# Performance work log

Hardware: AMD Instinct MI355X
Metric: run time of the kernel (lower is better)

## Reference

```python
import jax, jax.numpy as jnp
import numpy as np

T = 1024       # context time steps
F = 2048       # number of features (independent chains)
LATENT = 128   # latent_dim
ODE_H = 256    # ode_hidden_dim


def setup_inputs() -> dict:
    key = jax.random.key(0)
    ks = jax.random.split(key, 12)
    # strictly increasing observation times in [0, 100]
    context_times = jnp.sort(jax.random.uniform(ks[0], (T,), jnp.float32)) * 100.0
    context_values = jax.random.normal(ks[1], (T, F), jnp.float32)
    context_mask = (jax.random.uniform(ks[2], (T, F), jnp.float32) < 0.7).astype(jnp.float32)
    s = 0.05
    # EncoderODEFunc: Linear(LATENT->ODE_H), Tanh, Linear(ODE_H->LATENT)
    W1 = jax.random.normal(ks[3], (ODE_H, LATENT), jnp.float32) * s
    b1 = jax.random.normal(ks[4], (ODE_H,), jnp.float32) * s
    W2 = jax.random.normal(ks[5], (LATENT, ODE_H), jnp.float32) * s
    b2 = jax.random.normal(ks[6], (LATENT,), jnp.float32) * s
    # GRUCell(input_size=1, hidden_size=LATENT); torch gate order: r, z, n
    W_ih = jax.random.normal(ks[7], (3 * LATENT, 1), jnp.float32) * s
    b_ih = jax.random.normal(ks[8], (3 * LATENT,), jnp.float32) * s
    W_hh = jax.random.normal(ks[9], (3 * LATENT, LATENT), jnp.float32) * s
    b_hh = jax.random.normal(ks[10], (3 * LATENT,), jnp.float32) * s
    return {"context_times": context_times, "context_values": context_values,
            "context_mask": context_mask, "W1": W1, "b1": b1, "W2": W2, "b2": b2,
            "W_ih": W_ih, "b_ih": b_ih, "W_hh": W_hh, "b_hh": b_hh}


def reference(context_times, context_values, context_mask,
              W1, b1, W2, b2, W_ih, b_ih, W_hh, b_hh):
    latent = W_hh.shape[1]
    rev_t = context_times[::-1]
    rev_v = context_values[::-1]        # [T, F]
    rev_m = context_mask[::-1]          # [T, F]
    # dt for step k (k>=1) = rev_t[k-1] - rev_t[k]; step 0 has no ODE solve
    dts = jnp.concatenate([jnp.zeros((1,), rev_t.dtype), rev_t[:-1] - rev_t[1:]])

    def ode_f(h):  # [F, latent] -> [F, latent]
        return jnp.tanh(h @ W1.T + b1) @ W2.T + b2

    def gru_cell(x, h):  # x: [F, 1], h: [F, latent]
        gi = x @ W_ih.T + b_ih          # [F, 3*latent]
        gh = h @ W_hh.T + b_hh
        ir, iz, inn = jnp.split(gi, 3, axis=-1)
        hr, hz, hn = jnp.split(gh, 3, axis=-1)
        r = jax.nn.sigmoid(ir + hr)
        z = jax.nn.sigmoid(iz + hz)
        n = jnp.tanh(inn + r * hn)
        return (1.0 - z) * n + z * h

    def step(h, inp):
        dt, obs, m = inp
        # single fixed Euler step over [0, dt] (torchdiffeq odeint, method='euler')
        h_ode = h + dt * ode_f(h)
        h = jnp.where(dt > 0.0, h_ode, h)
        h_cand = gru_cell(obs[:, None], h)
        m = m[:, None]
        return m * h_cand + (1.0 - m) * h, None

    h0 = jnp.zeros((context_values.shape[-1], latent), context_values.dtype)
    h, _ = jax.lax.scan(step, h0, (dts, rev_v, rev_m))
    return h  # [F, latent] == z0
```

## Files before the change

kernel.cpp:

```cpp
#include <hip/hip_runtime.h>

#define T_STEPS 1024
#define FDIM    2048
#define LAT     128
#define HID     256
#define MB      8
#define NTHR    512
#define NBLK    (FDIM / MB)

typedef __attribute__((ext_vector_type(8))) short bf16x8;
typedef __attribute__((ext_vector_type(4))) float f32x4;

#define L2E  1.4426950408889634f
#define C2E  2.8853900817779268f

__device__ __forceinline__ float exp2_(float x) {
#if __has_builtin(__builtin_amdgcn_exp2f)
    return __builtin_amdgcn_exp2f(x);
#else
    return __expf(0.6931471805599453f * x);
#endif
}
__device__ __forceinline__ float rcp_(float x) { return __builtin_amdgcn_rcpf(x); }

__device__ __forceinline__ unsigned short f2bu(float x) {
    unsigned u = __float_as_uint(x);
    u += 0x7fffu + ((u >> 16) & 1u);
    return (unsigned short)(u >> 16);
}
__device__ __forceinline__ short f2b(float x) { return (short)f2bu(x); }
__device__ __forceinline__ unsigned pk2(float a, float b) {
    return (unsigned)f2bu(a) | ((unsigned)f2bu(b) << 16);
}
__device__ __forceinline__ float2 pick2(f32x4 v, int hf) {
    float a = hf ? v[2] : v[0];
    float b = hf ? v[3] : v[1];
    return make_float2(a, b);
}


__global__ __launch_bounds__(NTHR, 2)
void odernn_kernel(const float* __restrict__ times,
                   const float* __restrict__ vals,
                   const float* __restrict__ mask,
                   const float* __restrict__ W1,  const float* __restrict__ b1,
                   const float* __restrict__ W2,  const float* __restrict__ b2,
                   const float* __restrict__ W_ih, const float* __restrict__ b_ih,
                   const float* __restrict__ Whh, const float* __restrict__ b_hh,
                   float* __restrict__ out)
{
    __shared__ float dts_s[T_STEPS];
    __shared__ short hTpre[16 * 64];
    __shared__ short hTpost[16 * 64];
    __shared__ short uT[32 * 64];

    const int tid = threadIdx.x;
    const int w   = tid >> 6;
    const int ln  = tid & 63;
    const int col = ln & 15;
    const int qd  = ln >> 4;
    const int m8  = ln & 7;
    const int hf  = (ln >> 3) & 1;
    const int fbase = blockIdx.x * MB;
    const int rbase = qd * 64 + m8 * 8;

    for (int e = tid; e < T_STEPS; e += NTHR)
        dts_s[e] = (e == 0) ? 0.0f : (times[T_STEPS - e] - times[T_STEPS - 1 - e]);
    for (int e = tid; e < 16 * 64; e += NTHR) { hTpre[e] = 0; hTpost[e] = 0; }

    auto loadW = [&](const float* __restrict__ W, int K, int tb, int kb) -> bf16x8 {
        const float* p = W + (size_t)(tb + col) * K + kb * 32 + qd * 8;
        const float4 a = *(const float4*)p;
        const float4 b = *(const float4*)(p + 4);
        bf16x8 r;
        r[0] = f2b(a.x); r[1] = f2b(a.y); r[2] = f2b(a.z); r[3] = f2b(a.w);
        r[4] = f2b(b.x); r[5] = f2b(b.y); r[6] = f2b(b.z); r[7] = f2b(b.w);
        return r;
    };

    bf16x8 w1a[2][4];
    #pragma unroll
    for (int i = 0; i < 2; ++i)
        #pragma unroll
        for (int kb = 0; kb < 4; ++kb) w1a[i][kb] = loadW(W1, LAT, (2 * w + i) * 16, kb);
    bf16x8 w2a[8];
    #pragma unroll
    for (int kb = 0; kb < 8; ++kb) w2a[kb] = loadW(W2, HID, w * 16, kb);
    bf16x8 wha[3][4];
    #pragma unroll
    for (int g = 0; g < 3; ++g)
        #pragma unroll
        for (int kb = 0; kb < 4; ++kb)
            wha[g][kb] = loadW(Whh, LAT, g * 128 + w * 16, kb);

    float cb1L[2][2], b2L[2];
    float wrS[2], brS[2], wzS[2], bzS[2], wnC[2], bnC[2], bhnC[2];
    #pragma unroll
    for (int i = 0; i < 2; ++i)
        #pragma unroll
        for (int j = 0; j < 2; ++j)
            cb1L[i][j] = C2E * b1[(2 * w + i) * 16 + qd * 4 + hf * 2 + j];
    #pragma unroll
    for (int j = 0; j < 2; ++j) {
        const int c = w * 16 + qd * 4 + hf * 2 + j;
        b2L[j]  = b2[c];
        wrS[j]  = -L2E * W_ih[c];
        brS[j]  = -L2E * (b_ih[c] + b_hh[c]);
        wzS[j]  = -L2E * W_ih[128 + c];
        bzS[j]  = -L2E * (b_ih[128 + c] + b_hh[128 + c]);
        wnC[j]  =  C2E * W_ih[256 + c];
        bnC[j]  =  C2E * b_ih[256 + c];
        bhnC[j] =  C2E * b_hh[256 + c];
    }
    float hreg[2] = {0.f, 0.f};
    const int myAddr = (w * 2 + (qd >> 1)) * 64 + m8 * 8 + (qd & 1) * 4 + hf * 2;

    const float* vp = vals + (size_t)(T_STEPS - 1) * FDIM + fbase + m8;
    const float* mp = mask + (size_t)(T_STEPS - 1) * FDIM + fbase + m8;

    __syncthreads();

    for (int t = 0; t < T_STEPS; ++t) {
        const float dt = dts_s[t];
        const float x  = *vp;  vp -= FDIM;
        const float mk = *mp;  mp -= FDIM;

        f32x4 a1[2] = {{0,0,0,0},{0,0,0,0}};
        #pragma unroll
        for (int kb = 0; kb < 4; ++kb) {
            const bf16x8 bf = *(const bf16x8*)(hTpre + kb * 256 + rbase);
            #pragma unroll
            for (int i = 0; i < 2; ++i)
                a1[i] = __builtin_amdgcn_mfma_f32_16x16x32_bf16(w1a[i][kb], bf, a1[i], 0, 0, 0);
        }
        #pragma unroll
        for (int i = 0; i < 2; ++i) {
            const float2 p = pick2(a1[i], hf);
            const float v0 = fmaf(-2.f, rcp_(1.f + exp2_(fmaf(p.x, C2E, cb1L[i][0]))), 1.f);
            const float v1 = fmaf(-2.f, rcp_(1.f + exp2_(fmaf(p.y, C2E, cb1L[i][1]))), 1.f);
            const int addr = ((2 * w + i) * 2 + (qd >> 1)) * 64 + m8 * 8 + (qd & 1) * 4 + hf * 2;
            *(unsigned*)(uT + addr) = pk2(v0, v1);
        }
        __syncthreads();

        f32x4 a2a = {0,0,0,0}, a2b = {0,0,0,0};
        #pragma unroll
        for (int kb = 0; kb < 4; ++kb) {
            const bf16x8 bfa = *(const bf16x8*)(uT + kb * 256 + rbase);
            const bf16x8 bfb = *(const bf16x8*)(uT + (kb + 4) * 256 + rbase);
            a2a = __builtin_amdgcn_mfma_f32_16x16x32_bf16(w2a[kb],     bfa, a2a, 0, 0, 0);
            a2b = __builtin_amdgcn_mfma_f32_16x16x32_bf16(w2a[kb + 4], bfb, a2b, 0, 0, 0);
        }
        {
            const f32x4 a2 = a2a + a2b;
            const float2 p = pick2(a2, hf);
            hreg[0] = fmaf(dt, p.x + b2L[0], hreg[0]);
            hreg[1] = fmaf(dt, p.y + b2L[1], hreg[1]);
            *(unsigned*)(hTpost + myAddr) = pk2(hreg[0], hreg[1]);
        }
        __syncthreads();

        f32x4 a3[3] = {{0,0,0,0},{0,0,0,0},{0,0,0,0}};
        #pragma unroll
        for (int kb = 0; kb < 4; ++kb) {
            const bf16x8 bf = *(const bf16x8*)(hTpost + kb * 256 + rbase);
            #pragma unroll
            for (int g = 0; g < 3; ++g)
                a3[g] = __builtin_amdgcn_mfma_f32_16x16x32_bf16(wha[g][kb], bf, a3[g], 0, 0, 0);
        }
        {
            const float2 gR = pick2(a3[0], hf);
            const float2 gZ = pick2(a3[1], hf);
            const float2 gN = pick2(a3[2], hf);
            const float gRv[2] = {gR.x, gR.y}, gZv[2] = {gZ.x, gZ.y}, gNv[2] = {gN.x, gN.y};
            #pragma unroll
            for (int j = 0; j < 2; ++j) {
                const float sr = rcp_(1.f + exp2_(fmaf(gRv[j], -L2E, fmaf(x, wrS[j], brS[j]))));
                const float sz = rcp_(1.f + exp2_(fmaf(gZv[j], -L2E, fmaf(x, wzS[j], bzS[j]))));
                const float yn = fmaf(sr, fmaf(gNv[j], C2E, bhnC[j]), fmaf(x, wnC[j], bnC[j]));
                const float nn = fmaf(-2.f, rcp_(1.f + exp2_(yn)), 1.f);
                const float hv = hreg[j];
                const float hc = fmaf(sz, hv - nn, nn);
                hreg[j] = fmaf(mk, hc - hv, hv);
            }
            *(unsigned*)(hTpre + myAddr) = pk2(hreg[0], hreg[1]);
        }
        __syncthreads();
    }

    {
        float2 o = make_float2(hreg[0], hreg[1]);
        *(float2*)(out + (size_t)(fbase + m8) * LAT + w * 16 + qd * 4 + hf * 2) = o;
    }
}

extern "C" void kernel_launch(void* const* d_in, const int* in_sizes, int n_in,
                              void* d_out, int out_size, void* d_ws, size_t ws_size,
                              hipStream_t stream) {
    const float* times = (const float*)d_in[0];
    const float* vals  = (const float*)d_in[1];
    const float* mask  = (const float*)d_in[2];
    const float* W1    = (const float*)d_in[3];
    const float* b1    = (const float*)d_in[4];
    const float* W2    = (const float*)d_in[5];
    const float* b2    = (const float*)d_in[6];
    const float* W_ih  = (const float*)d_in[7];
    const float* b_ih  = (const float*)d_in[8];
    const float* Whh   = (const float*)d_in[9];
    const float* b_hh  = (const float*)d_in[10];
    float* out = (float*)d_out;

    odernn_kernel<<<NBLK, NTHR, 0, stream>>>(times, vals, mask,
                                             W1, b1, W2, b2,
                                             W_ih, b_ih, Whh, b_hh, out);
}
```

Measured before the change: 1.124 ms.

## Halve waves per block and give each wave two output tiles

Cuts the block from 8 waves to 4 and has each wave compute twice as many 16-row tiles in every GEMM stage (W1, W2, W_hh). Weight fragments and per-column constants move into registers at twice the previous size. Launch bounds change to one block per SM. The aim is to cut barrier cost and wave count per serial time step and to give each wave more independent MFMAs to interleave. The cost is higher register pressure and fewer resident waves to hide latency.

```diff
diff --git a/kernel.cpp b/kernel.cpp
--- a/kernel.cpp
+++ b/kernel.cpp
@@ -5,7 +5,7 @@
 #define LAT     128
 #define HID     256
 #define MB      8
-#define NTHR    512
+#define NTHR    256
 #define NBLK    (FDIM / MB)
 
 typedef __attribute__((ext_vector_type(8))) short bf16x8;
@@ -39,7 +39,7 @@
 }
 
 
-__global__ __launch_bounds__(NTHR, 2)
+__global__ __launch_bounds__(NTHR, 1)
 void odernn_kernel(const float* __restrict__ times,
                    const float* __restrict__ vals,
                    const float* __restrict__ mask,
@@ -78,42 +78,51 @@
         return r;
     };
 
-    bf16x8 w1a[2][4];
+    bf16x8 w1a[4][4];
+    #pragma unroll
+    for (int i = 0; i < 4; ++i)
+        #pragma unroll
+        for (int kb = 0; kb < 4; ++kb) w1a[i][kb] = loadW(W1, LAT, (4 * w + i) * 16, kb);
+    bf16x8 w2a[2][8];
     #pragma unroll
     for (int i = 0; i < 2; ++i)
         #pragma unroll
-        for (int kb = 0; kb < 4; ++kb) w1a[i][kb] = loadW(W1, LAT, (2 * w + i) * 16, kb);
-    bf16x8 w2a[8];
-    #pragma unroll
-    for (int kb = 0; kb < 8; ++kb) w2a[kb] = loadW(W2, HID, w * 16, kb);
-    bf16x8 wha[3][4];
+        for (int kb = 0; kb < 8; ++kb) w2a[i][kb] = loadW(W2, HID, (2 * w + i) * 16, kb);
+    bf16x8 wha[3][2][4];
     #pragma unroll
     for (int g = 0; g < 3; ++g)
         #pragma unroll
-        for (int kb = 0; kb < 4; ++kb)
-            wha[g][kb] = loadW(Whh, LAT, g * 128 + w * 16, kb);
-
-    float cb1L[2][2], b2L[2];
-    float wrS[2], brS[2], wzS[2], bzS[2], wnC[2], bnC[2], bhnC[2];
+        for (int i = 0; i < 2; ++i)
+            #pragma unroll
+            for (int kb = 0; kb < 4; ++kb)
+                wha[g][i][kb] = loadW(Whh, LAT, g * 128 + (2 * w + i) * 16, kb);
+
+    float cb1L[4][2], b2L[2][2];
+    float wrS[2][2], brS[2][2], wzS[2][2], bzS[2][2], wnC[2][2], bnC[2][2], bhnC[2][2];
+    #pragma unroll
+    for (int i = 0; i < 4; ++i)
+        #pragma unroll
+        for (int j = 0; j < 2; ++j)
+            cb1L[i][j] = C2E * b1[(4 * w + i) * 16 + qd * 4 + hf * 2 + j];
     #pragma unroll
     for (int i = 0; i < 2; ++i)
         #pragma unroll
-        for (int j = 0; j < 2; ++j)
-            cb1L[i][j] = C2E * b1[(2 * w + i) * 16 + qd * 4 + hf * 2 + j];
-    #pragma unroll
-    for (int j = 0; j < 2; ++j) {
-        const int c = w * 16 + qd * 4 + hf * 2 + j;
-        b2L[j]  = b2[c];
-        wrS[j]  = -L2E * W_ih[c];
-        brS[j]  = -L2E * (b_ih[c] + b_hh[c]);
-        wzS[j]  = -L2E * W_ih[128 + c];
-        bzS[j]  = -L2E * (b_ih[128 + c] + b_hh[128 + c]);
-        wnC[j]  =  C2E * W_ih[256 + c];
-        bnC[j]  =  C2E * b_ih[256 + c];
-        bhnC[j] =  C2E * b_hh[256 + c];
-    }
-    float hreg[2] = {0.f, 0.f};
-    const int myAddr = (w * 2 + (qd >> 1)) * 64 + m8 * 8 + (qd & 1) * 4 + hf * 2;
+        for (int j = 0; j < 2; ++j) {
+            const int c = (2 * w + i) * 16 + qd * 4 + hf * 2 + j;
+            b2L[i][j]  = b2[c];
+            wrS[i][j]  = -L2E * W_ih[c];
+            brS[i][j]  = -L2E * (b_ih[c] + b_hh[c]);
+            wzS[i][j]  = -L2E * W_ih[128 + c];
+            bzS[i][j]  = -L2E * (b_ih[128 + c] + b_hh[128 + c]);
+            wnC[i][j]  =  C2E * W_ih[256 + c];
+            bnC[i][j]  =  C2E * b_ih[256 + c];
+            bhnC[i][j] =  C2E * b_hh[256 + c];
+        }
+    float hreg[2][2] = {{0.f, 0.f}, {0.f, 0.f}};
+    int myAddr[2];
+    #pragma unroll
+    for (int i = 0; i < 2; ++i)
+        myAddr[i] = ((2 * w + i) * 2 + (qd >> 1)) * 64 + m8 * 8 + (qd & 1) * 4 + hf * 2;
 
     const float* vp = vals + (size_t)(T_STEPS - 1) * FDIM + fbase + m8;
     const float* mp = mask + (size_t)(T_STEPS - 1) * FDIM + fbase + m8;
@@ -125,72 +134,80 @@
         const float x  = *vp;  vp -= FDIM;
         const float mk = *mp;  mp -= FDIM;
 
-        f32x4 a1[2] = {{0,0,0,0},{0,0,0,0}};
+        f32x4 a1[4] = {{0,0,0,0},{0,0,0,0},{0,0,0,0},{0,0,0,0}};
         #pragma unroll
         for (int kb = 0; kb < 4; ++kb) {
             const bf16x8 bf = *(const bf16x8*)(hTpre + kb * 256 + rbase);
             #pragma unroll
-            for (int i = 0; i < 2; ++i)
+            for (int i = 0; i < 4; ++i)
                 a1[i] = __builtin_amdgcn_mfma_f32_16x16x32_bf16(w1a[i][kb], bf, a1[i], 0, 0, 0);
         }
         #pragma unroll
-        for (int i = 0; i < 2; ++i) {
+        for (int i = 0; i < 4; ++i) {
             const float2 p = pick2(a1[i], hf);
             const float v0 = fmaf(-2.f, rcp_(1.f + exp2_(fmaf(p.x, C2E, cb1L[i][0]))), 1.f);
             const float v1 = fmaf(-2.f, rcp_(1.f + exp2_(fmaf(p.y, C2E, cb1L[i][1]))), 1.f);
-            const int addr = ((2 * w + i) * 2 + (qd >> 1)) * 64 + m8 * 8 + (qd & 1) * 4 + hf * 2;
+            const int addr = ((4 * w + i) * 2 + (qd >> 1)) * 64 + m8 * 8 + (qd & 1) * 4 + hf * 2;
             *(unsigned*)(uT + addr) = pk2(v0, v1);
         }
         __syncthreads();
 
-        f32x4 a2a = {0,0,0,0}, a2b = {0,0,0,0};
+        f32x4 a2a[2] = {{0,0,0,0},{0,0,0,0}}, a2b[2] = {{0,0,0,0},{0,0,0,0}};
         #pragma unroll
         for (int kb = 0; kb < 4; ++kb) {
             const bf16x8 bfa = *(const bf16x8*)(uT + kb * 256 + rbase);
             const bf16x8 bfb = *(const bf16x8*)(uT + (kb + 4) * 256 + rbase);
-            a2a = __builtin_amdgcn_mfma_f32_16x16x32_bf16(w2a[kb],     bfa, a2a, 0, 0, 0);
-            a2b = __builtin_amdgcn_mfma_f32_16x16x32_bf16(w2a[kb + 4], bfb, a2b, 0, 0, 0);
-        }
-        {
-            const f32x4 a2 = a2a + a2b;
+            #pragma unroll
+            for (int i = 0; i < 2; ++i) {
+                a2a[i] = __builtin_amdgcn_mfma_f32_16x16x32_bf16(w2a[i][kb],     bfa, a2a[i], 0, 0, 0);
+                a2b[i] = __builtin_amdgcn_mfma_f32_16x16x32_bf16(w2a[i][kb + 4], bfb, a2b[i], 0, 0, 0);
+            }
+        }
+        #pragma unroll
+        for (int i = 0; i < 2; ++i) {
+            const f32x4 a2 = a2a[i] + a2b[i];
             const float2 p = pick2(a2, hf);
-            hreg[0] = fmaf(dt, p.x + b2L[0], hreg[0]);
-            hreg[1] = fmaf(dt, p.y + b2L[1], hreg[1]);
-            *(unsigned*)(hTpost + myAddr) = pk2(hreg[0], hreg[1]);
+            hreg[i][0] = fmaf(dt, p.x + b2L[i][0], hreg[i][0]);
+            hreg[i][1] = fmaf(dt, p.y + b2L[i][1], hreg[i][1]);
+            *(unsigned*)(hTpost + myAddr[i]) = pk2(hreg[i][0], hreg[i][1]);
         }
         __syncthreads();
 
-        f32x4 a3[3] = {{0,0,0,0},{0,0,0,0},{0,0,0,0}};
+        f32x4 a3[3][2] = {{{0,0,0,0},{0,0,0,0}},{{0,0,0,0},{0,0,0,0}},{{0,0,0,0},{0,0,0,0}}};
         #pragma unroll
         for (int kb = 0; kb < 4; ++kb) {
             const bf16x8 bf = *(const bf16x8*)(hTpost + kb * 256 + rbase);
             #pragma unroll
             for (int g = 0; g < 3; ++g)
-                a3[g] = __builtin_amdgcn_mfma_f32_16x16x32_bf16(wha[g][kb], bf, a3[g], 0, 0, 0);
-        }
-        {
-            const float2 gR = pick2(a3[0], hf);
-            const float2 gZ = pick2(a3[1], hf);
-            const float2 gN = pick2(a3[2], hf);
+                #pragma unroll
+                for (int i = 0; i < 2; ++i)
+                    a3[g][i] = __builtin_amdgcn_mfma_f32_16x16x32_bf16(wha[g][i][kb], bf, a3[g][i], 0, 0, 0);
+        }
+        #pragma unroll
+        for (int i = 0; i < 2; ++i) {
+            const float2 gR = pick2(a3[0][i], hf);
+            const float2 gZ = pick2(a3[1][i], hf);
+            const float2 gN = pick2(a3[2][i], hf);
             const float gRv[2] = {gR.x, gR.y}, gZv[2] = {gZ.x, gZ.y}, gNv[2] = {gN.x, gN.y};
             #pragma unroll
             for (int j = 0; j < 2; ++j) {
-                const float sr = rcp_(1.f + exp2_(fmaf(gRv[j], -L2E, fmaf(x, wrS[j], brS[j]))));
-                const float sz = rcp_(1.f + exp2_(fmaf(gZv[j], -L2E, fmaf(x, wzS[j], bzS[j]))));
-                const float yn = fmaf(sr, fmaf(gNv[j], C2E, bhnC[j]), fmaf(x, wnC[j], bnC[j]));
+                const float sr = rcp_(1.f + exp2_(fmaf(gRv[j], -L2E, fmaf(x, wrS[i][j], brS[i][j]))));
+                const float sz = rcp_(1.f + exp2_(fmaf(gZv[j], -L2E, fmaf(x, wzS[i][j], bzS[i][j]))));
+                const float yn = fmaf(sr, fmaf(gNv[j], C2E, bhnC[i][j]), fmaf(x, wnC[i][j], bnC[i][j]));
                 const float nn = fmaf(-2.f, rcp_(1.f + exp2_(yn)), 1.f);
-                const float hv = hreg[j];
+                const float hv = hreg[i][j];
                 const float hc = fmaf(sz, hv - nn, nn);
-                hreg[j] = fmaf(mk, hc - hv, hv);
+                hreg[i][j] = fmaf(mk, hc - hv, hv);
             }
-            *(unsigned*)(hTpre + myAddr) = pk2(hreg[0], hreg[1]);
+            *(unsigned*)(hTpre + myAddr[i]) = pk2(hreg[i][0], hreg[i][1]);
         }
         __syncthreads();
     }
 
-    {
-        float2 o = make_float2(hreg[0], hreg[1]);
-        *(float2*)(out + (size_t)(fbase + m8) * LAT + w * 16 + qd * 4 + hf * 2) = o;
+    #pragma unroll
+    for (int i = 0; i < 2; ++i) {
+        float2 o = make_float2(hreg[i][0], hreg[i][1]);
+        *(float2*)(out + (size_t)(fbase + m8) * LAT + (2 * w + i) * 16 + qd * 4 + hf * 2) = o;
     }
 }
 
```

New measurement: 1.601 ms. 42.4% more time.

## Fold W_hh·W2 into precomputed fp8 matrix to remove one barrier per step

Applied to the files above, without the earlier changes.

Precomputes Wc = W_hh·W2 (scaled and stored as fp8 e4m3) and cb = W_hh·b2 in a small prep kernel. This allows the GRU hidden projection of h_ode to be computed as W_hh·h + dt·(Wc·u + cb) alongside the existing matmuls. The W_hh·h MFMAs now run in the first phase with W1, and the Wc·u fp8 MFMAs run in the second phase. The third matmul phase and one __syncthreads per time step are removed, shortening the serial dependency chain. It adds fp8 quantization error and more register pressure from the new weight fragments.

```diff
diff --git a/kernel.cpp b/kernel.cpp
--- a/kernel.cpp
+++ b/kernel.cpp
@@ -14,6 +14,12 @@
 #define L2E  1.4426950408889634f
 #define C2E  2.8853900817779268f
 
+#if defined(__has_builtin)
+# if __has_builtin(__builtin_amdgcn_cvt_pk_fp8_f32)
+#  define HAS_CVT_FP8 1
+# endif
+#endif
+
 __device__ __forceinline__ float exp2_(float x) {
 #if __has_builtin(__builtin_amdgcn_exp2f)
     return __builtin_amdgcn_exp2f(x);
@@ -36,6 +42,34 @@
     float a = hf ? v[2] : v[0];
     float b = hf ? v[3] : v[1];
     return make_float2(a, b);
+}
+
+__device__ __forceinline__ unsigned char enc_e4m3(float v) {
+    float av = fminf(fabsf(v), 448.0f);
+    const unsigned s = (__float_as_uint(v) >> 24) & 0x80u;
+    const unsigned ub = __float_as_uint(av);
+    const unsigned r  = ub + 0x7FFFFu + ((ub >> 20) & 1u);
+    const unsigned en = (r >> 20) - 960u;
+    const unsigned m  = (unsigned)__float2int_rn(av * 512.0f);
+    const unsigned code = (av >= 0.015625f) ? en : m;
+    return (unsigned char)(s | code);
+}
+
+__global__ void prep_wc(const float* __restrict__ Whh, const float* __restrict__ W2,
+                        const float* __restrict__ b2,
+                        unsigned char* __restrict__ wc8, float* __restrict__ cb)
+{
+    const int r = blockIdx.x;
+    const int c = threadIdx.x;
+    float acc = 0.0f;
+    for (int l = 0; l < LAT; ++l)
+        acc = fmaf(Whh[r * LAT + l], W2[l * HID + c], acc);
+    wc8[r * HID + c] = enc_e4m3(16.0f * acc);
+    if (c == 0) {
+        float a = 0.0f;
+        for (int l = 0; l < LAT; ++l) a = fmaf(Whh[r * LAT + l], b2[l], a);
+        cb[r] = a;
+    }
 }
 
 
@@ -47,12 +81,13 @@
                    const float* __restrict__ W2,  const float* __restrict__ b2,
                    const float* __restrict__ W_ih, const float* __restrict__ b_ih,
                    const float* __restrict__ Whh, const float* __restrict__ b_hh,
+                   const unsigned char* __restrict__ wc8, const float* __restrict__ cb,
                    float* __restrict__ out)
 {
     __shared__ float dts_s[T_STEPS];
     __shared__ short hTpre[16 * 64];
-    __shared__ short hTpost[16 * 64];
     __shared__ short uT[32 * 64];
+    __shared__ unsigned char uT8[32 * 64];
 
     const int tid = threadIdx.x;
     const int w   = tid >> 6;
@@ -66,7 +101,7 @@
 
     for (int e = tid; e < T_STEPS; e += NTHR)
         dts_s[e] = (e == 0) ? 0.0f : (times[T_STEPS - e] - times[T_STEPS - 1 - e]);
-    for (int e = tid; e < 16 * 64; e += NTHR) { hTpre[e] = 0; hTpost[e] = 0; }
+    for (int e = tid; e < 16 * 64; e += NTHR) hTpre[e] = 0;
 
     auto loadW = [&](const float* __restrict__ W, int K, int tb, int kb) -> bf16x8 {
         const float* p = W + (size_t)(tb + col) * K + kb * 32 + qd * 8;
@@ -83,17 +118,23 @@
     for (int i = 0; i < 2; ++i)
         #pragma unroll
         for (int kb = 0; kb < 4; ++kb) w1a[i][kb] = loadW(W1, LAT, (2 * w + i) * 16, kb);
-    bf16x8 w2a[8];
-    #pragma unroll
-    for (int kb = 0; kb < 8; ++kb) w2a[kb] = loadW(W2, HID, w * 16, kb);
     bf16x8 wha[3][4];
     #pragma unroll
     for (int g = 0; g < 3; ++g)
         #pragma unroll
         for (int kb = 0; kb < 4; ++kb)
             wha[g][kb] = loadW(Whh, LAT, g * 128 + w * 16, kb);
-
-    float cb1L[2][2], b2L[2];
+    bf16x8 w2a[8];
+    #pragma unroll
+    for (int kb = 0; kb < 8; ++kb) w2a[kb] = loadW(W2, HID, w * 16, kb);
+    long wca[3][8];
+    #pragma unroll
+    for (int g = 0; g < 3; ++g)
+        #pragma unroll
+        for (int kb = 0; kb < 8; ++kb)
+            wca[g][kb] = *(const long*)(wc8 + (size_t)(g * 128 + w * 16 + col) * HID + kb * 32 + qd * 8);
+
+    float cb1L[2][2], b2L[2], cbL[3][2];
     float wrS[2], brS[2], wzS[2], bzS[2], wnC[2], bnC[2], bhnC[2];
     #pragma unroll
     for (int i = 0; i < 2; ++i)
@@ -111,9 +152,12 @@
         wnC[j]  =  C2E * W_ih[256 + c];
         bnC[j]  =  C2E * b_ih[256 + c];
         bhnC[j] =  C2E * b_hh[256 + c];
+        #pragma unroll
+        for (int g = 0; g < 3; ++g) cbL[g][j] = cb[g * 128 + c];
     }
     float hreg[2] = {0.f, 0.f};
-    const int myAddr = (w * 2 + (qd >> 1)) * 64 + m8 * 8 + (qd & 1) * 4 + hf * 2;
+    const int grpBase = (w * 2 + (qd >> 1)) * 64 + m8 * 8 + (qd & 1) * 4 + hf * 2;
+    const int myAddr = grpBase;
 
     const float* vp = vals + (size_t)(T_STEPS - 1) * FDIM + fbase + m8;
     const float* mp = mask + (size_t)(T_STEPS - 1) * FDIM + fbase + m8;
@@ -124,26 +168,41 @@
         const float dt = dts_s[t];
         const float x  = *vp;  vp -= FDIM;
         const float mk = *mp;  mp -= FDIM;
+        const float mdt    = dt * (-L2E);
+        const float mdt16  = mdt * 0.0625f;
+        const float cdt    = dt * C2E;
+        const float cdt16  = cdt * 0.0625f;
 
         f32x4 a1[2] = {{0,0,0,0},{0,0,0,0}};
+        f32x4 g0[3] = {{0,0,0,0},{0,0,0,0},{0,0,0,0}};
         #pragma unroll
         for (int kb = 0; kb < 4; ++kb) {
             const bf16x8 bf = *(const bf16x8*)(hTpre + kb * 256 + rbase);
+            a1[0] = __builtin_amdgcn_mfma_f32_16x16x32_bf16(w1a[0][kb], bf, a1[0], 0, 0, 0);
+            a1[1] = __builtin_amdgcn_mfma_f32_16x16x32_bf16(w1a[1][kb], bf, a1[1], 0, 0, 0);
             #pragma unroll
-            for (int i = 0; i < 2; ++i)
-                a1[i] = __builtin_amdgcn_mfma_f32_16x16x32_bf16(w1a[i][kb], bf, a1[i], 0, 0, 0);
+            for (int g = 0; g < 3; ++g)
+                g0[g] = __builtin_amdgcn_mfma_f32_16x16x32_bf16(wha[g][kb], bf, g0[g], 0, 0, 0);
         }
         #pragma unroll
         for (int i = 0; i < 2; ++i) {
             const float2 p = pick2(a1[i], hf);
             const float v0 = fmaf(-2.f, rcp_(1.f + exp2_(fmaf(p.x, C2E, cb1L[i][0]))), 1.f);
             const float v1 = fmaf(-2.f, rcp_(1.f + exp2_(fmaf(p.y, C2E, cb1L[i][1]))), 1.f);
-            const int addr = ((2 * w + i) * 2 + (qd >> 1)) * 64 + m8 * 8 + (qd & 1) * 4 + hf * 2;
-            *(unsigned*)(uT + addr) = pk2(v0, v1);
+            const int ga = ((2 * w + i) * 2 + (qd >> 1)) * 64 + m8 * 8 + (qd & 1) * 4 + hf * 2;
+            *(unsigned*)(uT + ga) = pk2(v0, v1);
+#ifdef HAS_CVT_FP8
+            const int p8 = __builtin_amdgcn_cvt_pk_fp8_f32(v0, v1, 0, false);
+            *(unsigned short*)(uT8 + ga) = (unsigned short)(p8 & 0xffff);
+#else
+            *(unsigned short*)(uT8 + ga) =
+                (unsigned short)(enc_e4m3(v0) | ((unsigned)enc_e4m3(v1) << 8));
+#endif
         }
         __syncthreads();
 
         f32x4 a2a = {0,0,0,0}, a2b = {0,0,0,0};
+        f32x4 wc[3] = {{0,0,0,0},{0,0,0,0},{0,0,0,0}};
         #pragma unroll
         for (int kb = 0; kb < 4; ++kb) {
             const bf16x8 bfa = *(const bf16x8*)(uT + kb * 256 + rbase);
@@ -151,35 +210,37 @@
             a2a = __builtin_amdgcn_mfma_f32_16x16x32_bf16(w2a[kb],     bfa, a2a, 0, 0, 0);
             a2b = __builtin_amdgcn_mfma_f32_16x16x32_bf16(w2a[kb + 4], bfb, a2b, 0, 0, 0);
         }
+        #pragma unroll
+        for (int kb = 0; kb < 8; ++kb) {
+            const long u8 = *(const long*)(uT8 + (kb * 4 + qd) * 64 + m8 * 8);
+            #pragma unroll
+            for (int g = 0; g < 3; ++g)
+                wc[g] = __builtin_amdgcn_mfma_f32_16x16x32_fp8_fp8(wca[g][kb], u8, wc[g], 0, 0, 0);
+        }
         {
             const f32x4 a2 = a2a + a2b;
-            const float2 p = pick2(a2, hf);
-            hreg[0] = fmaf(dt, p.x + b2L[0], hreg[0]);
-            hreg[1] = fmaf(dt, p.y + b2L[1], hreg[1]);
-            *(unsigned*)(hTpost + myAddr) = pk2(hreg[0], hreg[1]);
-        }
-        __syncthreads();
-
-        f32x4 a3[3] = {{0,0,0,0},{0,0,0,0},{0,0,0,0}};
-        #pragma unroll
-        for (int kb = 0; kb < 4; ++kb) {
-            const bf16x8 bf = *(const bf16x8*)(hTpost + kb * 256 + rbase);
-            #pragma unroll
-            for (int g = 0; g < 3; ++g)
-                a3[g] = __builtin_amdgcn_mfma_f32_16x16x32_bf16(wha[g][kb], bf, a3[g], 0, 0, 0);
-        }
-        {
-            const float2 gR = pick2(a3[0], hf);
-            const float2 gZ = pick2(a3[1], hf);
-            const float2 gN = pick2(a3[2], hf);
-            const float gRv[2] = {gR.x, gR.y}, gZv[2] = {gZ.x, gZ.y}, gNv[2] = {gN.x, gN.y};
+            const float2 pw = pick2(a2, hf);
+            const float hp[2] = { fmaf(dt, pw.x + b2L[0], hreg[0]),
+                                  fmaf(dt, pw.y + b2L[1], hreg[1]) };
+            const float2 r0 = pick2(g0[0], hf), r1 = pick2(wc[0], hf);
+            const float2 z0 = pick2(g0[1], hf), z1 = pick2(wc[1], hf);
+            const float2 n0 = pick2(g0[2], hf), n1 = pick2(wc[2], hf);
+            const float g0r[2] = {r0.x, r0.y}, wcr[2] = {r1.x, r1.y};
+            const float g0z[2] = {z0.x, z0.y}, wcz[2] = {z1.x, z1.y};
+            const float g0n[2] = {n0.x, n0.y}, wcn[2] = {n1.x, n1.y};
             #pragma unroll
             for (int j = 0; j < 2; ++j) {
-                const float sr = rcp_(1.f + exp2_(fmaf(gRv[j], -L2E, fmaf(x, wrS[j], brS[j]))));
-                const float sz = rcp_(1.f + exp2_(fmaf(gZv[j], -L2E, fmaf(x, wzS[j], bzS[j]))));
-                const float yn = fmaf(sr, fmaf(gNv[j], C2E, bhnC[j]), fmaf(x, wnC[j], bnC[j]));
+                const float ar = fmaf(g0r[j], -L2E, fmaf(wcr[j], mdt16,
+                                   fmaf(cbL[0][j], mdt, fmaf(x, wrS[j], brS[j]))));
+                const float az = fmaf(g0z[j], -L2E, fmaf(wcz[j], mdt16,
+                                   fmaf(cbL[1][j], mdt, fmaf(x, wzS[j], bzS[j]))));
+                const float sr = rcp_(1.f + exp2_(ar));
+                const float sz = rcp_(1.f + exp2_(az));
+                const float gn2 = fmaf(g0n[j], C2E, fmaf(wcn[j], cdt16,
+                                    fmaf(cbL[2][j], cdt, bhnC[j])));
+                const float yn = fmaf(sr, gn2, fmaf(x, wnC[j], bnC[j]));
                 const float nn = fmaf(-2.f, rcp_(1.f + exp2_(yn)), 1.f);
-                const float hv = hreg[j];
+                const float hv = hp[j];
                 const float hc = fmaf(sz, hv - nn, nn);
                 hreg[j] = fmaf(mk, hc - hv, hv);
             }
@@ -210,7 +271,12 @@
     const float* b_hh  = (const float*)d_in[10];
     float* out = (float*)d_out;
 
+    unsigned char* wc8 = (unsigned char*)d_ws;
+    float*         cbp = (float*)((char*)d_ws + 98304);
+
+    prep_wc<<<384, 256, 0, stream>>>(Whh, W2, b2, wc8, cbp);
     odernn_kernel<<<NBLK, NTHR, 0, stream>>>(times, vals, mask,
                                              W1, b1, W2, b2,
-                                             W_ih, b_ih, Whh, b_hh, out);
-}
+                                             W_ih, b_ih, Whh, b_hh,
+                                             wc8, cbp, out);
+}
```

Result: slower. 1.444 ms (+28.4%).
